# Kernel tuning notes

Measured on AMD Instinct MI355X. Metric: run time of the kernel, lower is better.

## Reference

```python
import jax, jax.numpy as jnp
import numpy as np

BN_EPS = 1e-5

def _bn(x, g, b):
    # BatchNorm1d, training-mode batch statistics
    mu = x.mean(axis=0)
    var = x.var(axis=0)
    return g * (x - mu) / jnp.sqrt(var + BN_EPS) + b

def setup_inputs() -> dict:
    key = jax.random.key(0)
    ks = jax.random.split(key, 10)
    B2, D_in, D1, DIMS, C = 16384, 1024, 512, 256, 40
    B = B2 // 2
    def w(k, shape, fan_in):
        return jax.random.normal(k, shape, jnp.float32) / np.float32(np.sqrt(fan_in))
    return {
        "lufeat": jax.random.normal(ks[0], (B2, D_in), jnp.float32),
        "llabel": jax.random.randint(ks[1], (B,), 0, C),
        "W1": w(ks[2], (D_in, D1), D_in), "b1": jnp.zeros(D1, jnp.float32),
        "W2": w(ks[3], (D1, DIMS), D1), "b2": jnp.zeros(DIMS, jnp.float32),
        "W3": w(ks[4], (DIMS + C, 256), DIMS + C), "b3": jnp.zeros(256, jnp.float32),
        "W4": w(ks[5], (256, 64), 256), "b4": jnp.zeros(64, jnp.float32),
        "W5": w(ks[6], (64, 1), 64), "b5": jnp.zeros(1, jnp.float32),
        "g1": jnp.ones(256, jnp.float32), "be1": jnp.zeros(256, jnp.float32),
        "g2": jnp.ones(64, jnp.float32), "be2": jnp.zeros(64, jnp.float32),
        "mbank0": jax.random.normal(ks[7], (C, DIMS), jnp.float32),
        "start0": jnp.zeros(C, jnp.float32),
    }

def reference(lufeat, llabel, W1, b1, W2, b2, W3, b3, W4, b4, W5, b5,
              g1, be1, g2, be2, mbank0, start0):
    B = lufeat.shape[0] // 2
    h = (lufeat @ W1 + b1) @ W2 + b2            # [2B, dims]
    h = h / jnp.linalg.norm(h, axis=1, keepdims=True)
    lfeat, ufeat = h[:B], h[B:]

    # Sequential per-sample memory-bank scatter/EMA update (detached feats)
    lf_sg = jax.lax.stop_gradient(lfeat)
    def step(carry, xs):
        start, mbank = carry
        lab, feat = xs
        row = jnp.where(start[lab] == 0, feat, 0.9 * mbank[lab] + 0.1 * feat)
        return (start.at[lab].set(1.0), mbank.at[lab].set(row)), None
    (_, mbank), _ = jax.lax.scan(step, (start0, mbank0), (llabel, lf_sg))
    mbank = jax.lax.stop_gradient(mbank)

    # cdist retrieval: [B, C] euclidean distances
    lm = jnp.linalg.norm(lfeat[:, None, :] - mbank[None, :, :], axis=-1)
    lscores = lm.min(axis=-1)
    um = jnp.linalg.norm(ufeat[:, None, :] - mbank[None, :, :], axis=-1)

    uf = jnp.concatenate([ufeat, um], axis=-1)   # [B, dims + C]
    u = jax.nn.relu(_bn(uf @ W3 + b3, g1, be1))
    u = jax.nn.relu(_bn(u @ W4 + b4, g2, be2))   # dropout = identity (eval)
    uscores = u @ W5 + b5                        # [B, 1]
    return lscores, uscores, mbank
```

## Files before the change

kernel.cpp:

```cpp
#include <hip/hip_runtime.h>
#include <hip/hip_bf16.h>
#include <stdint.h>

typedef __attribute__((ext_vector_type(4))) float f32x4;
typedef __attribute__((ext_vector_type(8))) short s16x8;
typedef __attribute__((ext_vector_type(4))) unsigned short u16x4;
typedef __attribute__((ext_vector_type(4))) int i32x4;

#define B2T 16384
#define BH 8192
#define DIN 1024
#define DD1 512
#define DIMS 256
#define NC 40
#define CAPS 2048

__device__ __forceinline__ unsigned short f2b(float f) {
  unsigned int u = __builtin_bit_cast(unsigned int, f);
  u += 0x7FFFu + ((u >> 16) & 1u);
  return (unsigned short)(u >> 16);
}

__device__ __forceinline__ float b2f(unsigned short u) {
  return __builtin_bit_cast(float, ((unsigned int)u) << 16);
}

__device__ __forceinline__ void gload16(const void* g, void* l) {
  __builtin_amdgcn_global_load_lds(
      (const __attribute__((address_space(1))) void*)g,
      (__attribute__((address_space(3))) void*)l, 16, 0, 0);
}

__global__ __launch_bounds__(256) void prep_all(const float* __restrict__ W1,
                                                const float* __restrict__ W2,
                                                const float* __restrict__ b1,
                                                const float* __restrict__ b2,
                                                const float* __restrict__ W3,
                                                const float* __restrict__ W4,
                                                unsigned short* __restrict__ WeffT,
                                                float* __restrict__ beff,
                                                unsigned short* __restrict__ W3T,
                                                unsigned short* __restrict__ W4T,
                                                float* __restrict__ statz) {
  __shared__ float W1s[32][36];
  __shared__ float W2sT[32][36];
  int b = blockIdx.x, t = threadIdx.x;
  if (b < 256) {
    int k0 = (b & 31) * 32, n0 = (b >> 5) * 32;
    int nn = t & 31, kq = t >> 5;
    f32x4 acc = (f32x4){0.f, 0.f, 0.f, 0.f};
    for (int j0 = 0; j0 < DD1; j0 += 32) {
#pragma unroll
      for (int i = 0; i < 4; ++i) {
        int idx = t + 256 * i;
        int kk = idx >> 5, jj = idx & 31;
        W1s[kk][jj] = W1[(size_t)(k0 + kk) * DD1 + j0 + jj];
        W2sT[jj][kk] = W2[(size_t)(j0 + kk) * DIMS + n0 + jj];
      }
      __syncthreads();
#pragma unroll
      for (int jj4 = 0; jj4 < 8; ++jj4) {
        f32x4 w2 = *(const f32x4*)&W2sT[nn][jj4 * 4];
        f32x4 w1_0 = *(const f32x4*)&W1s[kq * 4 + 0][jj4 * 4];
        f32x4 w1_1 = *(const f32x4*)&W1s[kq * 4 + 1][jj4 * 4];
        f32x4 w1_2 = *(const f32x4*)&W1s[kq * 4 + 2][jj4 * 4];
        f32x4 w1_3 = *(const f32x4*)&W1s[kq * 4 + 3][jj4 * 4];
        acc[0] += w1_0[0] * w2[0] + w1_0[1] * w2[1] + w1_0[2] * w2[2] + w1_0[3] * w2[3];
        acc[1] += w1_1[0] * w2[0] + w1_1[1] * w2[1] + w1_1[2] * w2[2] + w1_1[3] * w2[3];
        acc[2] += w1_2[0] * w2[0] + w1_2[1] * w2[1] + w1_2[2] * w2[2] + w1_2[3] * w2[3];
        acc[3] += w1_3[0] * w2[0] + w1_3[1] * w2[1] + w1_3[2] * w2[2] + w1_3[3] * w2[3];
      }
      __syncthreads();
    }
    u16x4 pk = {f2b(acc[0]), f2b(acc[1]), f2b(acc[2]), f2b(acc[3])};
    *(u16x4*)(WeffT + (size_t)(n0 + nn) * DIN + k0 + kq * 4) = pk;
  } else if (b == 256) {
    float a0 = 0.f, a1 = 0.f, a2 = 0.f, a3 = 0.f, a4 = 0.f, a5 = 0.f, a6 = 0.f, a7 = 0.f;
    for (int j = 0; j < DD1; j += 8) {
      a0 += b1[j + 0] * W2[(size_t)(j + 0) * DIMS + t];
      a1 += b1[j + 1] * W2[(size_t)(j + 1) * DIMS + t];
      a2 += b1[j + 2] * W2[(size_t)(j + 2) * DIMS + t];
      a3 += b1[j + 3] * W2[(size_t)(j + 3) * DIMS + t];
      a4 += b1[j + 4] * W2[(size_t)(j + 4) * DIMS + t];
      a5 += b1[j + 5] * W2[(size_t)(j + 5) * DIMS + t];
      a6 += b1[j + 6] * W2[(size_t)(j + 6) * DIMS + t];
      a7 += b1[j + 7] * W2[(size_t)(j + 7) * DIMS + t];
    }
    beff[t] = b2[t] + (((a0 + a1) + (a2 + a3)) + ((a4 + a5) + (a6 + a7)));
  } else if (b < 577) {
    int idx = (b - 257) * 256 + t;
    int n = idx / 320, k = idx - n * 320;
    float v = (k < 296) ? W3[(size_t)k * 256 + n] : 0.0f;
    W3T[(size_t)n * 320 + k] = f2b(v);
  } else if (b < 641) {
    int idx = (b - 577) * 256 + t;
    int n = idx >> 8, k = idx & 255;
    W4T[(size_t)n * 256 + k] = f2b(W4[(size_t)k * 64 + n]);
  } else {
    for (int i = t; i < 640; i += 256) statz[i] = 0.0f;
  }
}

template <int AMODE, int NB, int MI, int CW, int EPI, int K, int TPB>
__global__ __launch_bounds__(TPB) void gemm_core(
    const void* __restrict__ Aptr, int lda, const unsigned short* __restrict__ BT,
    const float* __restrict__ bias, float* __restrict__ C, int ldc,
    float* __restrict__ sums, float* __restrict__ ssqs,
    const float* __restrict__ bnsum, const float* __restrict__ bnssq,
    const float* __restrict__ bng, const float* __restrict__ bnbe,
    unsigned short* __restrict__ uf) {
  constexpr int NW = TPB / 64;
  constexpr int RG = NW / CW;
  constexpr int AR = RG * MI * 16;
  constexpr int ACH = AR * 8;
  constexpr int ABN = (ACH + TPB - 1) / TPB;
  constexpr int BBN = NB * 8 / TPB;
  constexpr int BBUF = NB * 128;
  __shared__ __align__(16) short A_s[2][AR][72];
  __shared__ __align__(16) char B_s[2 * BBUF];
  __shared__ float rs[CW][AR];
  __shared__ float bsc_s[(AMODE == 2) ? 256 : 1];
  __shared__ float bsh_s[(AMODE == 2) ? 256 : 1];
  int t = threadIdx.x;
  int m0 = blockIdx.x * AR;
  int w = t >> 6, lane = t & 63, q = lane >> 4, ln = lane & 15;
  f32x4 acc[MI][4];
#pragma unroll
  for (int mi = 0; mi < MI; ++mi)
#pragma unroll
    for (int ni = 0; ni < 4; ++ni) acc[mi][ni] = (f32x4){0.f, 0.f, 0.f, 0.f};

  f32x4 pa0[ABN][2], pa1[ABN][2];
  s16x8 pab0[ABN], pab1[ABN];

  auto issueA = [&](int kbase, f32x4 (&paX)[ABN][2], s16x8 (&pabX)[ABN]) {
    if (ACH >= TPB || t < ACH) {
#pragma unroll
      for (int i = 0; i < ABN; ++i) {
        int ch = t + TPB * i, row = ch >> 3, kp = (ch & 7) * 8;
        if constexpr (AMODE == 1) {
          const unsigned short* A = (const unsigned short*)Aptr;
          pabX[i] = *(const s16x8*)(A + (size_t)(m0 + row) * lda + kbase + kp);
        } else {
          const float* A = (const float*)Aptr;
          const f32x4* src = (const f32x4*)(A + (size_t)(m0 + row) * lda + kbase + kp);
          paX[i][0] = src[0];
          paX[i][1] = src[1];
        }
      }
    }
  };

  auto gloadB = [&](int kbase, int bufi) {
#pragma unroll
    for (int i = 0; i < BBN; ++i) {
      int ch = t + TPB * i;
      int n = ch >> 3, j = ch & 7;
      int ksw = (j ^ (n & 7)) * 8;
      gload16(BT + (size_t)n * K + kbase + ksw,
              B_s + bufi * BBUF + (w * 64 + TPB * i) * 16);
    }
  };

  auto stageA = [&](int kk, int bufi, f32x4 (&paX)[ABN][2], s16x8 (&pabX)[ABN]) {
    if (ACH >= TPB || t < ACH) {
#pragma unroll
      for (int i = 0; i < ABN; ++i) {
        int ch = t + TPB * i, row = ch >> 3, kp = (ch & 7) * 8;
        if constexpr (AMODE == 1) {
          *(s16x8*)&A_s[bufi][row][kp] = pabX[i];
        } else {
          f32x4 v0 = paX[i][0], v1 = paX[i][1];
          if constexpr (AMODE == 2) {
            float vv[8] = {v0[0], v0[1], v0[2], v0[3], v1[0], v1[1], v1[2], v1[3]};
#pragma unroll
            for (int j = 0; j < 8; ++j) {
              int f = kk + kp + j;
              vv[j] = fmaxf(vv[j] * bsc_s[f] + bsh_s[f], 0.0f);
            }
            v0 = (f32x4){vv[0], vv[1], vv[2], vv[3]};
            v1 = (f32x4){vv[4], vv[5], vv[6], vv[7]};
          }
          s16x8 p;
          p[0] = (short)f2b(v0[0]); p[1] = (short)f2b(v0[1]);
          p[2] = (short)f2b(v0[2]); p[3] = (short)f2b(v0[3]);
          p[4] = (short)f2b(v1[0]); p[5] = (short)f2b(v1[1]);
          p[6] = (short)f2b(v1[2]); p[7] = (short)f2b(v1[3]);
          *(s16x8*)&A_s[bufi][row][kp] = p;
        }
      }
    }
  };

  auto compute = [&](int cur) {
#pragma unroll
    for (int k32 = 0; k32 < 64; k32 += 32) {
      s16x8 af[MI];
      int ab = (w / CW) * MI * 16;
#pragma unroll
      for (int mi = 0; mi < MI; ++mi)
        af[mi] = *(const s16x8*)&A_s[cur][ab + mi * 16 + ln][k32 + q * 8];
      int nb0 = (w % CW) * 64;
#pragma unroll
      for (int ni = 0; ni < 4; ++ni) {
        int brow = nb0 + ni * 16 + ln;
        int bb = (brow * 128 + (k32 + q * 8) * 2) ^ ((brow & 7) << 4);
        s16x8 bfr = *(const s16x8*)(B_s + cur * BBUF + bb);
#pragma unroll
        for (int mi = 0; mi < MI; ++mi)
          acc[mi][ni] = __builtin_amdgcn_mfma_f32_16x16x32_bf16(af[mi], bfr, acc[mi][ni], 0, 0, 0);
      }
    }
  };

  if constexpr (AMODE == 2) {
    if (t < 256) {
      float mu = bnsum[t] * (1.0f / 8192.0f);
      float var = bnssq[t] * (1.0f / 8192.0f) - mu * mu;
      float sc = bng[t] * rsqrtf(var + 1e-5f);
      bsc_s[t] = sc;
      bsh_s[t] = bnbe[t] - mu * sc;
    }
    __syncthreads();
  }

  const int nst = K >> 6;
  issueA(0, pa0, pab0);
  gloadB(0, 0);
  if (nst > 1) issueA(64, pa1, pab1);
  stageA(0, 0, pa0, pab0);
  __syncthreads();

  for (int s = 0; s < nst; s += 2) {
    if (s + 1 < nst) gloadB((s + 1) << 6, 1);
    if (s + 2 < nst) issueA((s + 2) << 6, pa0, pab0);
    compute(0);
    if (s + 1 < nst) stageA((s + 1) << 6, 1, pa1, pab1);
    __syncthreads();
    if (s + 1 < nst) {
      if (s + 2 < nst) gloadB((s + 2) << 6, 0);
      if (s + 3 < nst) issueA((s + 3) << 6, pa1, pab1);
      compute(1);
      if (s + 2 < nst) stageA((s + 2) << 6, 0, pa0, pab0);
      __syncthreads();
    }
  }

  float v[MI][4][4];
#pragma unroll
  for (int mi = 0; mi < MI; ++mi)
#pragma unroll
    for (int ni = 0; ni < 4; ++ni) {
      float bv = bias[(w % CW) * 64 + ni * 16 + ln];
#pragma unroll
      for (int r = 0; r < 4; ++r) v[mi][ni][r] = acc[mi][ni][r] + bv;
    }

  if constexpr (EPI == 1) {
    float p[MI][4];
#pragma unroll
    for (int mi = 0; mi < MI; ++mi)
#pragma unroll
      for (int r = 0; r < 4; ++r) {
        float s = v[mi][0][r] * v[mi][0][r] + v[mi][1][r] * v[mi][1][r] +
                  v[mi][2][r] * v[mi][2][r] + v[mi][3][r] * v[mi][3][r];
        s += __shfl_xor(s, 1); s += __shfl_xor(s, 2);
        s += __shfl_xor(s, 4); s += __shfl_xor(s, 8);
        p[mi][r] = s;
      }
    if (ln == 0) {
#pragma unroll
      for (int mi = 0; mi < MI; ++mi)
#pragma unroll
        for (int r = 0; r < 4; ++r)
          rs[w % CW][(w / CW) * MI * 16 + mi * 16 + q * 4 + r] = p[mi][r];
    }
    __syncthreads();
    if (t < AR) {
      float s = rs[0][t];
#pragma unroll
      for (int i = 1; i < CW; ++i) s += rs[i][t];
      rs[0][t] = rsqrtf(s);
    }
    __syncthreads();
#pragma unroll
    for (int mi = 0; mi < MI; ++mi)
#pragma unroll
      for (int r = 0; r < 4; ++r) {
        int ribf = (w / CW) * MI * 16 + mi * 16 + q * 4 + r;
        float inv = rs[0][ribf];
        int grow = m0 + ribf;
#pragma unroll
        for (int ni = 0; ni < 4; ++ni) {
          int col = (w % CW) * 64 + ni * 16 + ln;
          float nv = v[mi][ni][r] * inv;
          if (grow < BH)
            C[(size_t)grow * ldc + col] = nv;
          else
            uf[(size_t)(grow - BH) * 320 + col] = f2b(nv);
        }
      }
  } else {
#pragma unroll
    for (int mi = 0; mi < MI; ++mi)
#pragma unroll
      for (int ni = 0; ni < 4; ++ni)
#pragma unroll
        for (int r = 0; r < 4; ++r) {
          int grow = m0 + (w / CW) * MI * 16 + mi * 16 + q * 4 + r;
          int col = (w % CW) * 64 + ni * 16 + ln;
          C[(size_t)grow * ldc + col] = v[mi][ni][r];
        }
    if constexpr (EPI == 2 || EPI == 3) {
#pragma unroll
      for (int ni = 0; ni < 4; ++ni) {
        float s = 0.f, s2 = 0.f;
#pragma unroll
        for (int mi = 0; mi < MI; ++mi)
#pragma unroll
          for (int r = 0; r < 4; ++r) {
            float x = v[mi][ni][r];
            s += x; s2 += x * x;
          }
        s += __shfl_xor(s, 16); s += __shfl_xor(s, 32);
        s2 += __shfl_xor(s2, 16); s2 += __shfl_xor(s2, 32);
        if (q == 0) {
          int col = (w % CW) * 64 + ni * 16 + ln;
          atomicAdd(&sums[col], s);
          atomicAdd(&ssqs[col], s2);
        }
      }
    }
  }
}

__global__ __launch_bounds__(256) void bank_kernel(const int* __restrict__ llabel,
                                                   const float* __restrict__ Hn,
                                                   const float* __restrict__ mbank0,
                                                   const float* __restrict__ start0,
                                                   float* __restrict__ mbank_out,
                                                   float* __restrict__ msq) {
  __shared__ i32x4 lab4[BH / 4];
  __shared__ int idx_s[CAPS];
  __shared__ int wcnt[4];
  __shared__ float red[4];
  int t = threadIdx.x, c = blockIdx.x;
  int w = t >> 6, lane = t & 63;

  for (int i = t; i < BH / 4; i += 256) lab4[i] = ((const i32x4*)llabel)[i];
  __syncthreads();
  const int* lab_s = (const int*)lab4;

  int base0 = w * (BH / 4);
  int cnt = 0;
  for (int b = 0; b < BH / 4; b += 64)
    cnt += (int)__popcll(__ballot(lab_s[base0 + b + lane] == c));
  if (lane == 0) wcnt[w] = cnt;
  __syncthreads();
  int off = 0;
#pragma unroll
  for (int i = 0; i < 4; ++i)
    if (i < w) off += wcnt[i];
  int Ktot = wcnt[0] + wcnt[1] + wcnt[2] + wcnt[3];

  int running = off;
  for (int b = 0; b < BH / 4; b += 64) {
    bool hit = lab_s[base0 + b + lane] == c;
    unsigned long long mk = __ballot(hit);
    if (hit) {
      int pos = running + (int)__popcll(mk & ((1ull << lane) - 1ull));
      if (pos < CAPS) idx_s[pos] = base0 + b + lane;
    }
    running += (int)__popcll(mk);
  }
  __syncthreads();
  int K = Ktot < CAPS ? Ktot : CAPS;

  const float l09 = -0.15200309344504997f;
  bool fresh = (start0[c] == 0.0f);
  float out;
  if (K == 0) {
    out = mbank0[(size_t)c * DIMS + t];
  } else {
    float a0 = 0.f, a1 = 0.f, a2 = 0.f, a3 = 0.f, a4 = 0.f, a5 = 0.f, a6 = 0.f, a7 = 0.f;
    float w0fold = fresh ? exp2f((float)K * l09) : 0.f;
    int m = 0;
    for (; m + 8 <= K; m += 8) {
      float e = (float)(K - 1 - m);
      float wa = 0.1f * exp2f(e * l09) + (m == 0 ? w0fold : 0.f);
      a0 += wa * Hn[(size_t)idx_s[m + 0] * DIMS + t];
      a1 += 0.1f * exp2f((e - 1.f) * l09) * Hn[(size_t)idx_s[m + 1] * DIMS + t];
      a2 += 0.1f * exp2f((e - 2.f) * l09) * Hn[(size_t)idx_s[m + 2] * DIMS + t];
      a3 += 0.1f * exp2f((e - 3.f) * l09) * Hn[(size_t)idx_s[m + 3] * DIMS + t];
      a4 += 0.1f * exp2f((e - 4.f) * l09) * Hn[(size_t)idx_s[m + 4] * DIMS + t];
      a5 += 0.1f * exp2f((e - 5.f) * l09) * Hn[(size_t)idx_s[m + 5] * DIMS + t];
      a6 += 0.1f * exp2f((e - 6.f) * l09) * Hn[(size_t)idx_s[m + 6] * DIMS + t];
      a7 += 0.1f * exp2f((e - 7.f) * l09) * Hn[(size_t)idx_s[m + 7] * DIMS + t];
    }
    for (; m < K; ++m) {
      float wa = 0.1f * exp2f((float)(K - 1 - m) * l09) + (m == 0 ? w0fold : 0.f);
      a0 += wa * Hn[(size_t)idx_s[m] * DIMS + t];
    }
    float acc = ((a0 + a1) + (a2 + a3)) + ((a4 + a5) + (a6 + a7));
    float base_v = fresh ? 0.f : exp2f((float)K * l09) * mbank0[(size_t)c * DIMS + t];
    out = acc + base_v;
  }
  mbank_out[(size_t)c * DIMS + t] = out;
  float vv = out * out;
#pragma unroll
  for (int o = 32; o; o >>= 1) vv += __shfl_xor(vv, o);
  if ((t & 63) == 0) red[t >> 6] = vv;
  __syncthreads();
  if (t == 0) msq[c] = (red[0] + red[1]) + (red[2] + red[3]);
}

__global__ __launch_bounds__(256) void dist_kernel(const float* __restrict__ Hn,
                                                   const float* __restrict__ mbank,
                                                   const float* __restrict__ msq,
                                                   float* __restrict__ lscores,
                                                   unsigned short* __restrict__ uf) {
  __shared__ float Ms[NC][260];
  __shared__ float Hs[32][260];
  __shared__ float msq_s[NC];
  int t = threadIdx.x;
  int r0 = blockIdx.x * 32;
  for (int e = t; e < NC * 64; e += 256) {
    int i = e >> 6, d0 = (e & 63) * 4;
    *(f32x4*)&Ms[i][d0] = *(const f32x4*)(mbank + (size_t)i * DIMS + d0);
  }
  if (r0 < BH) {
    for (int e = t; e < 32 * 64; e += 256) {
      int i = e >> 6, d0 = (e & 63) * 4;
      *(f32x4*)&Hs[i][d0] = *(const f32x4*)(Hn + (size_t)(r0 + i) * DIMS + d0);
    }
  } else {
    for (int e = t; e < 32 * 32; e += 256) {
      int i = e >> 5, d0 = (e & 31) * 8;
      s16x8 vb = *(const s16x8*)(uf + (size_t)(r0 - BH + i) * 320 + d0);
#pragma unroll
      for (int j = 0; j < 8; ++j) Hs[i][d0 + j] = b2f((unsigned short)vb[j]);
    }
  }
  if (t < NC) msq_s[t] = msq[t];
  __syncthreads();
  int r = t >> 3, c0 = (t & 7) * 5;
  float g0 = 0, g1 = 0, g2 = 0, g3 = 0, g4 = 0;
  for (int d = 0; d < DIMS; d += 4) {
    f32x4 f = *(const f32x4*)&Hs[r][d];
    f32x4 m0v = *(const f32x4*)&Ms[c0 + 0][d];
    f32x4 m1v = *(const f32x4*)&Ms[c0 + 1][d];
    f32x4 m2v = *(const f32x4*)&Ms[c0 + 2][d];
    f32x4 m3v = *(const f32x4*)&Ms[c0 + 3][d];
    f32x4 m4v = *(const f32x4*)&Ms[c0 + 4][d];
    g0 += f[0] * m0v[0] + f[1] * m0v[1] + f[2] * m0v[2] + f[3] * m0v[3];
    g1 += f[0] * m1v[0] + f[1] * m1v[1] + f[2] * m1v[2] + f[3] * m1v[3];
    g2 += f[0] * m2v[0] + f[1] * m2v[1] + f[2] * m2v[2] + f[3] * m2v[3];
    g3 += f[0] * m3v[0] + f[1] * m3v[1] + f[2] * m3v[2] + f[3] * m3v[3];
    g4 += f[0] * m4v[0] + f[1] * m4v[1] + f[2] * m4v[2] + f[3] * m4v[3];
  }
  int row = r0 + r;
  float d2[5];
  d2[0] = 1.0f + msq_s[c0 + 0] - 2.0f * g0;
  d2[1] = 1.0f + msq_s[c0 + 1] - 2.0f * g1;
  d2[2] = 1.0f + msq_s[c0 + 2] - 2.0f * g2;
  d2[3] = 1.0f + msq_s[c0 + 3] - 2.0f * g3;
  d2[4] = 1.0f + msq_s[c0 + 4] - 2.0f * g4;
  if (row < BH) {
    float mn = fminf(fminf(fminf(d2[0], d2[1]), fminf(d2[2], d2[3])), d2[4]);
    mn = fminf(mn, __shfl_xor(mn, 1, 8));
    mn = fminf(mn, __shfl_xor(mn, 2, 8));
    mn = fminf(mn, __shfl_xor(mn, 4, 8));
    if ((t & 7) == 0) lscores[row] = sqrtf(fmaxf(mn, 0.0f));
  } else {
    unsigned short* dst = uf + (size_t)(row - BH) * 320 + 256 + c0;
#pragma unroll
    for (int qq = 0; qq < 5; ++qq) dst[qq] = f2b(sqrtf(fmaxf(d2[qq], 0.0f)));
  }
}

__global__ __launch_bounds__(256) void uscore_bn(const float* __restrict__ y2,
                                                 const float* __restrict__ sums2,
                                                 const float* __restrict__ ssqs2,
                                                 const float* __restrict__ g2,
                                                 const float* __restrict__ be2,
                                                 const float* __restrict__ W5,
                                                 const float* __restrict__ b5,
                                                 float* __restrict__ out) {
  int t = threadIdx.x;
  int wv = t >> 6, lane = t & 63;
  int row = blockIdx.x * 4 + wv;
  float mu = sums2[lane] * (1.0f / 8192.0f);
  float var = ssqs2[lane] * (1.0f / 8192.0f) - mu * mu;
  float sc = g2[lane] * rsqrtf(var + 1e-5f);
  float sh = be2[lane] - mu * sc;
  float v = fmaxf(y2[(size_t)row * 64 + lane] * sc + sh, 0.0f) * W5[lane];
#pragma unroll
  for (int o = 32; o; o >>= 1) v += __shfl_xor(v, o);
  if (lane == 0) out[row] = v + b5[0];
}

extern "C" void kernel_launch(void* const* d_in, const int* in_sizes, int n_in,
                              void* d_out, int out_size, void* d_ws, size_t ws_size,
                              hipStream_t stream) {
  const float* lufeat = (const float*)d_in[0];
  const int* llabel = (const int*)d_in[1];
  const float* W1 = (const float*)d_in[2];
  const float* b1 = (const float*)d_in[3];
  const float* W2 = (const float*)d_in[4];
  const float* b2 = (const float*)d_in[5];
  const float* W3 = (const float*)d_in[6];
  const float* b3 = (const float*)d_in[7];
  const float* W4 = (const float*)d_in[8];
  const float* b4 = (const float*)d_in[9];
  const float* W5 = (const float*)d_in[10];
  const float* b5 = (const float*)d_in[11];
  const float* g1 = (const float*)d_in[12];
  const float* be1 = (const float*)d_in[13];
  const float* g2 = (const float*)d_in[14];
  const float* be2 = (const float*)d_in[15];
  const float* mbank0 = (const float*)d_in[16];
  const float* start0 = (const float*)d_in[17];

  char* ws = (char*)d_ws;
  unsigned short* WeffT = (unsigned short*)(ws + 0);
  float* Hraw = (float*)(ws + 524288);
  float* ybuf = (float*)(ws + 524288);
  float* y2 = (float*)(ws + 8912896);
  unsigned short* uf = (unsigned short*)(ws + 17301504);
  unsigned short* W3T = (unsigned short*)(ws + 22544384);
  unsigned short* W4T = (unsigned short*)(ws + 22708224);
  float* beff = (float*)(ws + 22740992);
  float* sums1 = (float*)(ws + 22742016);
  float* ssq1 = sums1 + 256;
  float* sums2 = ssq1 + 256;
  float* ssq2 = sums2 + 64;
  float* msq = (float*)(ws + 22744576);

  float* lscores = (float*)d_out;
  float* uscores = lscores + 8192;
  float* mbank = uscores + 8192;

  prep_all<<<642, 256, 0, stream>>>(W1, W2, b1, b2, W3, W4, WeffT, beff, W3T, W4T, sums1);
  gemm_core<0, 256, 2, 4, 1, 1024, 256><<<512, 256, 0, stream>>>(
      lufeat, 1024, WeffT, beff, Hraw, 256,
      nullptr, nullptr, nullptr, nullptr, nullptr, nullptr, uf);
  bank_kernel<<<NC, 256, 0, stream>>>(llabel, Hraw, mbank0, start0, mbank, msq);
  dist_kernel<<<512, 256, 0, stream>>>(Hraw, mbank, msq, lscores, uf);
  gemm_core<1, 256, 1, 4, 2, 320, 512><<<256, 512, 0, stream>>>(
      uf, 320, W3T, b3, ybuf, 256,
      sums1, ssq1, nullptr, nullptr, nullptr, nullptr, nullptr);
  gemm_core<2, 64, 1, 1, 3, 256, 256><<<128, 256, 0, stream>>>(
      ybuf, 256, W4T, b4, y2, 64,
      sums2, ssq2, sums1, ssq1, g1, be1, nullptr);
  uscore_bn<<<2048, 256, 0, stream>>>(y2, sums2, ssq2, g2, be2, W5, b5, uscores);
}
```

Before: 238.0 us.

## Fuse post-GEMM stages into one persistent kernel with software grid barriers

Replaces the bank, distance, W3 GEMM, W4 GEMM and score kernels with a single 512-block persistent kernel that separates phases with an atomic grid barrier. The memory-bank EMA is parallelised over 4 dimension quarters per class, and BatchNorm statistics move from float atomics to per-block partials reduced in a dedicated phase. The aim is to remove several kernel launch gaps and tail effects. In exchange it adds grid-wide spin barriers, and it relies on all 512 blocks being co-resident, which is not guaranteed.

```diff
diff --git a/kernel.cpp b/kernel.cpp
--- a/kernel.cpp
+++ b/kernel.cpp
@@ -14,6 +14,7 @@
 #define DIMS 256
 #define NC 40
 #define CAPS 2048
+#define NBLK 512u
 
 __device__ __forceinline__ unsigned short f2b(float f) {
   unsigned int u = __builtin_bit_cast(unsigned int, f);
@@ -29,6 +30,23 @@
   __builtin_amdgcn_global_load_lds(
       (const __attribute__((address_space(1))) void*)g,
       (__attribute__((address_space(3))) void*)l, 16, 0, 0);
+}
+
+__device__ __forceinline__ void gridbar(unsigned* bar) {
+  __syncthreads();
+  if (threadIdx.x == 0) {
+    unsigned gen = __hip_atomic_load(bar + 1, __ATOMIC_RELAXED, __HIP_MEMORY_SCOPE_AGENT);
+    __threadfence();
+    if (atomicAdd(bar, 1u) == NBLK - 1u) {
+      __hip_atomic_store(bar, 0u, __ATOMIC_RELAXED, __HIP_MEMORY_SCOPE_AGENT);
+      __hip_atomic_store(bar + 1, gen + 1u, __ATOMIC_RELEASE, __HIP_MEMORY_SCOPE_AGENT);
+    } else {
+      while (__hip_atomic_load(bar + 1, __ATOMIC_ACQUIRE, __HIP_MEMORY_SCOPE_AGENT) == gen)
+        __builtin_amdgcn_s_sleep(8);
+    }
+    __threadfence();
+  }
+  __syncthreads();
 }
 
 __global__ __launch_bounds__(256) void prep_all(const float* __restrict__ W1,
@@ -97,7 +115,7 @@
     int n = idx >> 8, k = idx & 255;
     W4T[(size_t)n * 256 + k] = f2b(W4[(size_t)k * 64 + n]);
   } else {
-    for (int i = t; i < 640; i += 256) statz[i] = 0.0f;
+    for (int i = t; i < 688; i += 256) statz[i] = 0.0f;
   }
 }
 
@@ -119,8 +137,6 @@
   __shared__ __align__(16) short A_s[2][AR][72];
   __shared__ __align__(16) char B_s[2 * BBUF];
   __shared__ float rs[CW][AR];
-  __shared__ float bsc_s[(AMODE == 2) ? 256 : 1];
-  __shared__ float bsh_s[(AMODE == 2) ? 256 : 1];
   int t = threadIdx.x;
   int m0 = blockIdx.x * AR;
   int w = t >> 6, lane = t & 63, q = lane >> 4, ln = lane & 15;
@@ -133,7 +149,7 @@
   f32x4 pa0[ABN][2], pa1[ABN][2];
   s16x8 pab0[ABN], pab1[ABN];
 
-  auto issueA = [&](int kbase, f32x4 (&paX)[ABN][2], s16x8 (&pabX)[ABN]) {
+  auto issue = [&](int kbase, f32x4 (&paX)[ABN][2], s16x8 (&pabX)[ABN]) {
     if (ACH >= TPB || t < ACH) {
 #pragma unroll
       for (int i = 0; i < ABN; ++i) {
@@ -162,7 +178,7 @@
     }
   };
 
-  auto stageA = [&](int kk, int bufi, f32x4 (&paX)[ABN][2], s16x8 (&pabX)[ABN]) {
+  auto stage = [&](int bufi, f32x4 (&paX)[ABN][2], s16x8 (&pabX)[ABN]) {
     if (ACH >= TPB || t < ACH) {
 #pragma unroll
       for (int i = 0; i < ABN; ++i) {
@@ -171,16 +187,6 @@
           *(s16x8*)&A_s[bufi][row][kp] = pabX[i];
         } else {
           f32x4 v0 = paX[i][0], v1 = paX[i][1];
-          if constexpr (AMODE == 2) {
-            float vv[8] = {v0[0], v0[1], v0[2], v0[3], v1[0], v1[1], v1[2], v1[3]};
-#pragma unroll
-            for (int j = 0; j < 8; ++j) {
-              int f = kk + kp + j;
-              vv[j] = fmaxf(vv[j] * bsc_s[f] + bsh_s[f], 0.0f);
-            }
-            v0 = (f32x4){vv[0], vv[1], vv[2], vv[3]};
-            v1 = (f32x4){vv[4], vv[5], vv[6], vv[7]};
-          }
           s16x8 p;
           p[0] = (short)f2b(v0[0]); p[1] = (short)f2b(v0[1]);
           p[2] = (short)f2b(v0[2]); p[3] = (short)f2b(v0[3]);
@@ -213,35 +219,24 @@
     }
   };
 
-  if constexpr (AMODE == 2) {
-    if (t < 256) {
-      float mu = bnsum[t] * (1.0f / 8192.0f);
-      float var = bnssq[t] * (1.0f / 8192.0f) - mu * mu;
-      float sc = bng[t] * rsqrtf(var + 1e-5f);
-      bsc_s[t] = sc;
-      bsh_s[t] = bnbe[t] - mu * sc;
-    }
-    __syncthreads();
-  }
-
   const int nst = K >> 6;
-  issueA(0, pa0, pab0);
+  issue(0, pa0, pab0);
   gloadB(0, 0);
-  if (nst > 1) issueA(64, pa1, pab1);
-  stageA(0, 0, pa0, pab0);
+  if (nst > 1) issue(64, pa1, pab1);
+  stage(0, pa0, pab0);
   __syncthreads();
 
   for (int s = 0; s < nst; s += 2) {
     if (s + 1 < nst) gloadB((s + 1) << 6, 1);
-    if (s + 2 < nst) issueA((s + 2) << 6, pa0, pab0);
+    if (s + 2 < nst) issue((s + 2) << 6, pa0, pab0);
     compute(0);
-    if (s + 1 < nst) stageA((s + 1) << 6, 1, pa1, pab1);
+    if (s + 1 < nst) stage(1, pa1, pab1);
     __syncthreads();
     if (s + 1 < nst) {
       if (s + 2 < nst) gloadB((s + 2) << 6, 0);
-      if (s + 3 < nst) issueA((s + 3) << 6, pa1, pab1);
+      if (s + 3 < nst) issue((s + 3) << 6, pa1, pab1);
       compute(1);
-      if (s + 2 < nst) stageA((s + 2) << 6, 0, pa0, pab0);
+      if (s + 2 < nst) stage(0, pa0, pab0);
       __syncthreads();
     }
   }
@@ -300,203 +295,386 @@
             uf[(size_t)(grow - BH) * 320 + col] = f2b(nv);
         }
       }
-  } else {
-#pragma unroll
-    for (int mi = 0; mi < MI; ++mi)
-#pragma unroll
-      for (int ni = 0; ni < 4; ++ni)
-#pragma unroll
-        for (int r = 0; r < 4; ++r) {
-          int grow = m0 + (w / CW) * MI * 16 + mi * 16 + q * 4 + r;
-          int col = (w % CW) * 64 + ni * 16 + ln;
-          C[(size_t)grow * ldc + col] = v[mi][ni][r];
+  }
+}
+
+__global__ __launch_bounds__(256, 2) void fused_back(
+    const int* llabel, const float* Hn, const float* mbank0, const float* start0,
+    float* mbank, float* msq, float* lscores, unsigned short* uf,
+    const unsigned short* W3T, const float* b3, float* ybuf, float* part1,
+    float* bnsc1, float* bnsh1, const float* g1, const float* be1,
+    const unsigned short* W4T, const float* b4, float* y2, float* part2,
+    float* bnsc2, float* bnsh2, const float* g2, const float* be2,
+    const float* W5, const float* b5, float* uscores, unsigned* bar) {
+  __shared__ __align__(16) char smem[75264];
+  const int t = threadIdx.x;
+  const int w = t >> 6, lane = t & 63, q = lane >> 4, ln = lane & 15;
+  const int bx = blockIdx.x;
+  const float l09 = -0.15200309344504997f;
+
+  if (bx < 160) {
+    int c = bx >> 2, dq = bx & 3;
+    int* lab_s = (int*)smem;
+    int* idx_s = (int*)(smem + 32768);
+    float* redp = (float*)(smem + 40960);
+    int* wcnt = (int*)(smem + 41984);
+    for (int i = t; i < BH / 4; i += 256) ((i32x4*)lab_s)[i] = ((const i32x4*)llabel)[i];
+    __syncthreads();
+    int base0 = w * (BH / 4);
+    int cnt = 0;
+    for (int b = 0; b < BH / 4; b += 64)
+      cnt += (int)__popcll(__ballot(lab_s[base0 + b + lane] == c));
+    if (lane == 0) wcnt[w] = cnt;
+    __syncthreads();
+    int off = 0;
+#pragma unroll
+    for (int i = 0; i < 4; ++i)
+      if (i < w) off += wcnt[i];
+    int Ktot = wcnt[0] + wcnt[1] + wcnt[2] + wcnt[3];
+    int running = off;
+    for (int b = 0; b < BH / 4; b += 64) {
+      bool hit = lab_s[base0 + b + lane] == c;
+      unsigned long long mk = __ballot(hit);
+      if (hit) {
+        int pos = running + (int)__popcll(mk & ((1ull << lane) - 1ull));
+        if (pos < CAPS) idx_s[pos] = base0 + b + lane;
+      }
+      running += (int)__popcll(mk);
+    }
+    __syncthreads();
+    int K = Ktot < CAPS ? Ktot : CAPS;
+    bool fresh = (start0[c] == 0.0f);
+    int dcol = t & 63, rr = t >> 6;
+    int d = dq * 64 + dcol;
+    float p0 = 0.f, p1 = 0.f, p2 = 0.f, p3 = 0.f;
+    if (K > 0) {
+      float w0fold = fresh ? exp2f((float)K * l09) : 0.f;
+      int m = rr;
+      for (; m + 12 < K; m += 16) {
+        float e = (float)(K - 1 - m);
+        float wa = 0.1f * exp2f(e * l09) + (m == 0 ? w0fold : 0.f);
+        p0 += wa * Hn[(size_t)idx_s[m] * DIMS + d];
+        p1 += 0.1f * exp2f((e - 4.f) * l09) * Hn[(size_t)idx_s[m + 4] * DIMS + d];
+        p2 += 0.1f * exp2f((e - 8.f) * l09) * Hn[(size_t)idx_s[m + 8] * DIMS + d];
+        p3 += 0.1f * exp2f((e - 12.f) * l09) * Hn[(size_t)idx_s[m + 12] * DIMS + d];
+      }
+      for (; m < K; m += 4) {
+        float wa = 0.1f * exp2f((float)(K - 1 - m) * l09) + (m == 0 ? w0fold : 0.f);
+        p0 += wa * Hn[(size_t)idx_s[m] * DIMS + d];
+      }
+    }
+    redp[rr * 64 + dcol] = (p0 + p1) + (p2 + p3);
+    __syncthreads();
+    if (t < 64) {
+      int dd = dq * 64 + t;
+      float out;
+      if (K == 0) {
+        out = mbank0[(size_t)c * DIMS + dd];
+      } else {
+        float base_v = fresh ? 0.f : exp2f((float)K * l09) * mbank0[(size_t)c * DIMS + dd];
+        out = ((redp[t] + redp[64 + t]) + (redp[128 + t] + redp[192 + t])) + base_v;
+      }
+      mbank[(size_t)c * DIMS + dd] = out;
+      float vv = out * out;
+#pragma unroll
+      for (int o = 32; o; o >>= 1) vv += __shfl_xor(vv, o);
+      if (t == 0) atomicAdd(&msq[c], vv);
+    }
+  }
+  gridbar(bar);
+
+  {
+    float* Ms = (float*)smem;
+    float* Hs = (float*)(smem + 41600);
+    float* msq_s = (float*)(smem + 74880);
+    int r0 = bx * 32;
+    for (int e = t; e < NC * 64; e += 256) {
+      int i = e >> 6, d0 = (e & 63) * 4;
+      *(f32x4*)&Ms[i * 260 + d0] = *(const f32x4*)(mbank + (size_t)i * DIMS + d0);
+    }
+    if (r0 < BH) {
+      for (int e = t; e < 32 * 64; e += 256) {
+        int i = e >> 6, d0 = (e & 63) * 4;
+        *(f32x4*)&Hs[i * 260 + d0] = *(const f32x4*)(Hn + (size_t)(r0 + i) * DIMS + d0);
+      }
+    } else {
+      for (int e = t; e < 32 * 32; e += 256) {
+        int i = e >> 5, d0 = (e & 31) * 8;
+        s16x8 vb = *(const s16x8*)(uf + (size_t)(r0 - BH + i) * 320 + d0);
+#pragma unroll
+        for (int jj = 0; jj < 8; ++jj) Hs[i * 260 + d0 + jj] = b2f((unsigned short)vb[jj]);
+      }
+    }
+    if (t < NC) msq_s[t] = msq[t];
+    __syncthreads();
+    int r = t >> 3, c0 = (t & 7) * 5;
+    float g0 = 0, g1v = 0, g2v = 0, g3 = 0, g4 = 0;
+    for (int d = 0; d < DIMS; d += 4) {
+      f32x4 f = *(const f32x4*)&Hs[r * 260 + d];
+      f32x4 m0v = *(const f32x4*)&Ms[(c0 + 0) * 260 + d];
+      f32x4 m1v = *(const f32x4*)&Ms[(c0 + 1) * 260 + d];
+      f32x4 m2v = *(const f32x4*)&Ms[(c0 + 2) * 260 + d];
+      f32x4 m3v = *(const f32x4*)&Ms[(c0 + 3) * 260 + d];
+      f32x4 m4v = *(const f32x4*)&Ms[(c0 + 4) * 260 + d];
+      g0 += f[0] * m0v[0] + f[1] * m0v[1] + f[2] * m0v[2] + f[3] * m0v[3];
+      g1v += f[0] * m1v[0] + f[1] * m1v[1] + f[2] * m1v[2] + f[3] * m1v[3];
+      g2v += f[0] * m2v[0] + f[1] * m2v[1] + f[2] * m2v[2] + f[3] * m2v[3];
+      g3 += f[0] * m3v[0] + f[1] * m3v[1] + f[2] * m3v[2] + f[3] * m3v[3];
+      g4 += f[0] * m4v[0] + f[1] * m4v[1] + f[2] * m4v[2] + f[3] * m4v[3];
+    }
+    int row = r0 + r;
+    float d2[5];
+    d2[0] = 1.0f + msq_s[c0 + 0] - 2.0f * g0;
+    d2[1] = 1.0f + msq_s[c0 + 1] - 2.0f * g1v;
+    d2[2] = 1.0f + msq_s[c0 + 2] - 2.0f * g2v;
+    d2[3] = 1.0f + msq_s[c0 + 3] - 2.0f * g3;
+    d2[4] = 1.0f + msq_s[c0 + 4] - 2.0f * g4;
+    if (row < BH) {
+      float mn = fminf(fminf(fminf(d2[0], d2[1]), fminf(d2[2], d2[3])), d2[4]);
+      mn = fminf(mn, __shfl_xor(mn, 1, 8));
+      mn = fminf(mn, __shfl_xor(mn, 2, 8));
+      mn = fminf(mn, __shfl_xor(mn, 4, 8));
+      if ((t & 7) == 0) lscores[row] = sqrtf(fmaxf(mn, 0.0f));
+    } else {
+      unsigned short* dst = uf + (size_t)(row - BH) * 320 + 256 + c0;
+#pragma unroll
+      for (int qq = 0; qq < 5; ++qq) dst[qq] = f2b(sqrtf(fmaxf(d2[qq], 0.0f)));
+    }
+  }
+  gridbar(bar);
+
+  {
+    short* A_s = (short*)smem;
+    char* Bb = smem + 4608;
+    int m0 = bx * 16;
+    f32x4 acc[4];
+#pragma unroll
+    for (int ni = 0; ni < 4; ++ni) acc[ni] = (f32x4){0.f, 0.f, 0.f, 0.f};
+    s16x8 pA0, pA1;
+    auto issueA2 = [&](int kbase, s16x8& p) {
+      if (t < 128) {
+        int row = t >> 3, kp = (t & 7) * 8;
+        p = *(const s16x8*)(uf + (size_t)(m0 + row) * 320 + kbase + kp);
+      }
+    };
+    auto stageA2 = [&](int bufi, s16x8& p) {
+      if (t < 128) {
+        int row = t >> 3, kp = (t & 7) * 8;
+        *(s16x8*)&A_s[(bufi * 16 + row) * 72 + kp] = p;
+      }
+    };
+    auto gloadB2 = [&](int kbase, int bufi) {
+#pragma unroll
+      for (int i = 0; i < 8; ++i) {
+        int ch = t + 256 * i;
+        int n = ch >> 3, j = ch & 7;
+        int ksw = (j ^ (n & 7)) * 8;
+        gload16(W3T + (size_t)n * 320 + kbase + ksw, Bb + bufi * 32768 + ch * 16);
+      }
+    };
+    auto compute2 = [&](int cur) {
+#pragma unroll
+      for (int k32 = 0; k32 < 64; k32 += 32) {
+        s16x8 af = *(const s16x8*)&A_s[(cur * 16 + ln) * 72 + k32 + q * 8];
+#pragma unroll
+        for (int ni = 0; ni < 4; ++ni) {
+          int brow = w * 64 + ni * 16 + ln;
+          int bb = (brow * 128 + (k32 + q * 8) * 2) ^ ((brow & 7) << 4);
+          s16x8 bfr = *(const s16x8*)(Bb + cur * 32768 + bb);
+          acc[ni] = __builtin_amdgcn_mfma_f32_16x16x32_bf16(af, bfr, acc[ni], 0, 0, 0);
         }
-    if constexpr (EPI == 2 || EPI == 3) {
-#pragma unroll
-      for (int ni = 0; ni < 4; ++ni) {
-        float s = 0.f, s2 = 0.f;
-#pragma unroll
-        for (int mi = 0; mi < MI; ++mi)
-#pragma unroll
-          for (int r = 0; r < 4; ++r) {
-            float x = v[mi][ni][r];
-            s += x; s2 += x * x;
-          }
-        s += __shfl_xor(s, 16); s += __shfl_xor(s, 32);
-        s2 += __shfl_xor(s2, 16); s2 += __shfl_xor(s2, 32);
-        if (q == 0) {
-          int col = (w % CW) * 64 + ni * 16 + ln;
-          atomicAdd(&sums[col], s);
-          atomicAdd(&ssqs[col], s2);
+      }
+    };
+    issueA2(0, pA0); gloadB2(0, 0); issueA2(64, pA1); stageA2(0, pA0);
+    __syncthreads();
+    for (int s = 0; s < 5; s += 2) {
+      if (s + 1 < 5) gloadB2((s + 1) << 6, 1);
+      if (s + 2 < 5) issueA2((s + 2) << 6, pA0);
+      compute2(0);
+      if (s + 1 < 5) stageA2(1, pA1);
+      __syncthreads();
+      if (s + 1 < 5) {
+        if (s + 2 < 5) gloadB2((s + 2) << 6, 0);
+        if (s + 3 < 5) issueA2((s + 3) << 6, pA1);
+        compute2(1);
+        if (s + 2 < 5) stageA2(0, pA0);
+        __syncthreads();
+      }
+    }
+#pragma unroll
+    for (int ni = 0; ni < 4; ++ni) {
+      int col = w * 64 + ni * 16 + ln;
+      float bv = b3[col];
+      float s = 0.f, s2 = 0.f;
+#pragma unroll
+      for (int r = 0; r < 4; ++r) {
+        float x = acc[ni][r] + bv;
+        ybuf[(size_t)(m0 + q * 4 + r) * 256 + col] = x;
+        s += x; s2 += x * x;
+      }
+      s += __shfl_xor(s, 16); s += __shfl_xor(s, 32);
+      s2 += __shfl_xor(s2, 16); s2 += __shfl_xor(s2, 32);
+      if (q == 0) {
+        part1[col * 512 + bx] = s;
+        part1[131072 + col * 512 + bx] = s2;
+      }
+    }
+  }
+  gridbar(bar);
+
+  if (bx < 256) {
+    float* red = (float*)smem;
+    float s = part1[bx * 512 + t] + part1[bx * 512 + 256 + t];
+    float s2 = part1[131072 + bx * 512 + t] + part1[131072 + bx * 512 + 256 + t];
+#pragma unroll
+    for (int o = 32; o; o >>= 1) { s += __shfl_xor(s, o); s2 += __shfl_xor(s2, o); }
+    if (lane == 0) { red[w] = s; red[4 + w] = s2; }
+    __syncthreads();
+    if (t == 0) {
+      float S = (red[0] + red[1]) + (red[2] + red[3]);
+      float S2 = (red[4] + red[5]) + (red[6] + red[7]);
+      float mu = S * (1.0f / 8192.0f);
+      float var = S2 * (1.0f / 8192.0f) - mu * mu;
+      float sc = g1[bx] * rsqrtf(var + 1e-5f);
+      bnsc1[bx] = sc;
+      bnsh1[bx] = be1[bx] - mu * sc;
+    }
+  }
+  gridbar(bar);
+
+  if (bx < 128) {
+    short* A_s = (short*)smem;
+    char* Bb = smem + 18432;
+    float* bsc_s = (float*)(smem + 34816);
+    float* bsh_s = (float*)(smem + 35840);
+    bsc_s[t] = bnsc1[t];
+    bsh_s[t] = bnsh1[t];
+    __syncthreads();
+    int m0 = bx * 64;
+    f32x4 acc[4];
+#pragma unroll
+    for (int ni = 0; ni < 4; ++ni) acc[ni] = (f32x4){0.f, 0.f, 0.f, 0.f};
+    f32x4 pa0[2][2], pa1[2][2];
+    auto issueA3 = [&](int kbase, f32x4 (&pa)[2][2]) {
+#pragma unroll
+      for (int i = 0; i < 2; ++i) {
+        int ch = t + 256 * i, row = ch >> 3, kp = (ch & 7) * 8;
+        const f32x4* src = (const f32x4*)(ybuf + (size_t)(m0 + row) * 256 + kbase + kp);
+        pa[i][0] = src[0];
+        pa[i][1] = src[1];
+      }
+    };
+    auto stageA3 = [&](int kbase, int bufi, f32x4 (&pa)[2][2]) {
+#pragma unroll
+      for (int i = 0; i < 2; ++i) {
+        int ch = t + 256 * i, row = ch >> 3, kp = (ch & 7) * 8;
+        float vv[8] = {pa[i][0][0], pa[i][0][1], pa[i][0][2], pa[i][0][3],
+                       pa[i][1][0], pa[i][1][1], pa[i][1][2], pa[i][1][3]};
+#pragma unroll
+        for (int j = 0; j < 8; ++j) {
+          int f = kbase + kp + j;
+          vv[j] = fmaxf(vv[j] * bsc_s[f] + bsh_s[f], 0.0f);
         }
-      }
-    }
-  }
-}
-
-__global__ __launch_bounds__(256) void bank_kernel(const int* __restrict__ llabel,
-                                                   const float* __restrict__ Hn,
-                                                   const float* __restrict__ mbank0,
-                                                   const float* __restrict__ start0,
-                                                   float* __restrict__ mbank_out,
-                                                   float* __restrict__ msq) {
-  __shared__ i32x4 lab4[BH / 4];
-  __shared__ int idx_s[CAPS];
-  __shared__ int wcnt[4];
-  __shared__ float red[4];
-  int t = threadIdx.x, c = blockIdx.x;
-  int w = t >> 6, lane = t & 63;
-
-  for (int i = t; i < BH / 4; i += 256) lab4[i] = ((const i32x4*)llabel)[i];
-  __syncthreads();
-  const int* lab_s = (const int*)lab4;
-
-  int base0 = w * (BH / 4);
-  int cnt = 0;
-  for (int b = 0; b < BH / 4; b += 64)
-    cnt += (int)__popcll(__ballot(lab_s[base0 + b + lane] == c));
-  if (lane == 0) wcnt[w] = cnt;
-  __syncthreads();
-  int off = 0;
-#pragma unroll
-  for (int i = 0; i < 4; ++i)
-    if (i < w) off += wcnt[i];
-  int Ktot = wcnt[0] + wcnt[1] + wcnt[2] + wcnt[3];
-
-  int running = off;
-  for (int b = 0; b < BH / 4; b += 64) {
-    bool hit = lab_s[base0 + b + lane] == c;
-    unsigned long long mk = __ballot(hit);
-    if (hit) {
-      int pos = running + (int)__popcll(mk & ((1ull << lane) - 1ull));
-      if (pos < CAPS) idx_s[pos] = base0 + b + lane;
-    }
-    running += (int)__popcll(mk);
-  }
-  __syncthreads();
-  int K = Ktot < CAPS ? Ktot : CAPS;
-
-  const float l09 = -0.15200309344504997f;
-  bool fresh = (start0[c] == 0.0f);
-  float out;
-  if (K == 0) {
-    out = mbank0[(size_t)c * DIMS + t];
-  } else {
-    float a0 = 0.f, a1 = 0.f, a2 = 0.f, a3 = 0.f, a4 = 0.f, a5 = 0.f, a6 = 0.f, a7 = 0.f;
-    float w0fold = fresh ? exp2f((float)K * l09) : 0.f;
-    int m = 0;
-    for (; m + 8 <= K; m += 8) {
-      float e = (float)(K - 1 - m);
-      float wa = 0.1f * exp2f(e * l09) + (m == 0 ? w0fold : 0.f);
-      a0 += wa * Hn[(size_t)idx_s[m + 0] * DIMS + t];
-      a1 += 0.1f * exp2f((e - 1.f) * l09) * Hn[(size_t)idx_s[m + 1] * DIMS + t];
-      a2 += 0.1f * exp2f((e - 2.f) * l09) * Hn[(size_t)idx_s[m + 2] * DIMS + t];
-      a3 += 0.1f * exp2f((e - 3.f) * l09) * Hn[(size_t)idx_s[m + 3] * DIMS + t];
-      a4 += 0.1f * exp2f((e - 4.f) * l09) * Hn[(size_t)idx_s[m + 4] * DIMS + t];
-      a5 += 0.1f * exp2f((e - 5.f) * l09) * Hn[(size_t)idx_s[m + 5] * DIMS + t];
-      a6 += 0.1f * exp2f((e - 6.f) * l09) * Hn[(size_t)idx_s[m + 6] * DIMS + t];
-      a7 += 0.1f * exp2f((e - 7.f) * l09) * Hn[(size_t)idx_s[m + 7] * DIMS + t];
-    }
-    for (; m < K; ++m) {
-      float wa = 0.1f * exp2f((float)(K - 1 - m) * l09) + (m == 0 ? w0fold : 0.f);
-      a0 += wa * Hn[(size_t)idx_s[m] * DIMS + t];
-    }
-    float acc = ((a0 + a1) + (a2 + a3)) + ((a4 + a5) + (a6 + a7));
-    float base_v = fresh ? 0.f : exp2f((float)K * l09) * mbank0[(size_t)c * DIMS + t];
-    out = acc + base_v;
-  }
-  mbank_out[(size_t)c * DIMS + t] = out;
-  float vv = out * out;
-#pragma unroll
-  for (int o = 32; o; o >>= 1) vv += __shfl_xor(vv, o);
-  if ((t & 63) == 0) red[t >> 6] = vv;
-  __syncthreads();
-  if (t == 0) msq[c] = (red[0] + red[1]) + (red[2] + red[3]);
-}
-
-__global__ __launch_bounds__(256) void dist_kernel(const float* __restrict__ Hn,
-                                                   const float* __restrict__ mbank,
-                                                   const float* __restrict__ msq,
-                                                   float* __restrict__ lscores,
-                                                   unsigned short* __restrict__ uf) {
-  __shared__ float Ms[NC][260];
-  __shared__ float Hs[32][260];
-  __shared__ float msq_s[NC];
-  int t = threadIdx.x;
-  int r0 = blockIdx.x * 32;
-  for (int e = t; e < NC * 64; e += 256) {
-    int i = e >> 6, d0 = (e & 63) * 4;
-    *(f32x4*)&Ms[i][d0] = *(const f32x4*)(mbank + (size_t)i * DIMS + d0);
-  }
-  if (r0 < BH) {
-    for (int e = t; e < 32 * 64; e += 256) {
-      int i = e >> 6, d0 = (e & 63) * 4;
-      *(f32x4*)&Hs[i][d0] = *(const f32x4*)(Hn + (size_t)(r0 + i) * DIMS + d0);
-    }
-  } else {
-    for (int e = t; e < 32 * 32; e += 256) {
-      int i = e >> 5, d0 = (e & 31) * 8;
-      s16x8 vb = *(const s16x8*)(uf + (size_t)(r0 - BH + i) * 320 + d0);
-#pragma unroll
-      for (int j = 0; j < 8; ++j) Hs[i][d0 + j] = b2f((unsigned short)vb[j]);
-    }
-  }
-  if (t < NC) msq_s[t] = msq[t];
-  __syncthreads();
-  int r = t >> 3, c0 = (t & 7) * 5;
-  float g0 = 0, g1 = 0, g2 = 0, g3 = 0, g4 = 0;
-  for (int d = 0; d < DIMS; d += 4) {
-    f32x4 f = *(const f32x4*)&Hs[r][d];
-    f32x4 m0v = *(const f32x4*)&Ms[c0 + 0][d];
-    f32x4 m1v = *(const f32x4*)&Ms[c0 + 1][d];
-    f32x4 m2v = *(const f32x4*)&Ms[c0 + 2][d];
-    f32x4 m3v = *(const f32x4*)&Ms[c0 + 3][d];
-    f32x4 m4v = *(const f32x4*)&Ms[c0 + 4][d];
-    g0 += f[0] * m0v[0] + f[1] * m0v[1] + f[2] * m0v[2] + f[3] * m0v[3];
-    g1 += f[0] * m1v[0] + f[1] * m1v[1] + f[2] * m1v[2] + f[3] * m1v[3];
-    g2 += f[0] * m2v[0] + f[1] * m2v[1] + f[2] * m2v[2] + f[3] * m2v[3];
-    g3 += f[0] * m3v[0] + f[1] * m3v[1] + f[2] * m3v[2] + f[3] * m3v[3];
-    g4 += f[0] * m4v[0] + f[1] * m4v[1] + f[2] * m4v[2] + f[3] * m4v[3];
-  }
-  int row = r0 + r;
-  float d2[5];
-  d2[0] = 1.0f + msq_s[c0 + 0] - 2.0f * g0;
-  d2[1] = 1.0f + msq_s[c0 + 1] - 2.0f * g1;
-  d2[2] = 1.0f + msq_s[c0 + 2] - 2.0f * g2;
-  d2[3] = 1.0f + msq_s[c0 + 3] - 2.0f * g3;
-  d2[4] = 1.0f + msq_s[c0 + 4] - 2.0f * g4;
-  if (row < BH) {
-    float mn = fminf(fminf(fminf(d2[0], d2[1]), fminf(d2[2], d2[3])), d2[4]);
-    mn = fminf(mn, __shfl_xor(mn, 1, 8));
-    mn = fminf(mn, __shfl_xor(mn, 2, 8));
-    mn = fminf(mn, __shfl_xor(mn, 4, 8));
-    if ((t & 7) == 0) lscores[row] = sqrtf(fmaxf(mn, 0.0f));
-  } else {
-    unsigned short* dst = uf + (size_t)(row - BH) * 320 + 256 + c0;
-#pragma unroll
-    for (int qq = 0; qq < 5; ++qq) dst[qq] = f2b(sqrtf(fmaxf(d2[qq], 0.0f)));
-  }
-}
-
-__global__ __launch_bounds__(256) void uscore_bn(const float* __restrict__ y2,
-                                                 const float* __restrict__ sums2,
-                                                 const float* __restrict__ ssqs2,
-                                                 const float* __restrict__ g2,
-                                                 const float* __restrict__ be2,
-                                                 const float* __restrict__ W5,
-                                                 const float* __restrict__ b5,
-                                                 float* __restrict__ out) {
-  int t = threadIdx.x;
-  int wv = t >> 6, lane = t & 63;
-  int row = blockIdx.x * 4 + wv;
-  float mu = sums2[lane] * (1.0f / 8192.0f);
-  float var = ssqs2[lane] * (1.0f / 8192.0f) - mu * mu;
-  float sc = g2[lane] * rsqrtf(var + 1e-5f);
-  float sh = be2[lane] - mu * sc;
-  float v = fmaxf(y2[(size_t)row * 64 + lane] * sc + sh, 0.0f) * W5[lane];
-#pragma unroll
-  for (int o = 32; o; o >>= 1) v += __shfl_xor(v, o);
-  if (lane == 0) out[row] = v + b5[0];
+        s16x8 p;
+        p[0] = (short)f2b(vv[0]); p[1] = (short)f2b(vv[1]);
+        p[2] = (short)f2b(vv[2]); p[3] = (short)f2b(vv[3]);
+        p[4] = (short)f2b(vv[4]); p[5] = (short)f2b(vv[5]);
+        p[6] = (short)f2b(vv[6]); p[7] = (short)f2b(vv[7]);
+        *(s16x8*)&A_s[(bufi * 64 + row) * 72 + kp] = p;
+      }
+    };
+    auto gloadB3 = [&](int kbase, int bufi) {
+#pragma unroll
+      for (int i = 0; i < 2; ++i) {
+        int ch = t + 256 * i, n = ch >> 3, j = ch & 7;
+        int ksw = (j ^ (n & 7)) * 8;
+        gload16(W4T + (size_t)n * 256 + kbase + ksw, Bb + bufi * 8192 + ch * 16);
+      }
+    };
+    auto compute3 = [&](int cur) {
+#pragma unroll
+      for (int k32 = 0; k32 < 64; k32 += 32) {
+        s16x8 af = *(const s16x8*)&A_s[(cur * 64 + w * 16 + ln) * 72 + k32 + q * 8];
+#pragma unroll
+        for (int ni = 0; ni < 4; ++ni) {
+          int brow = ni * 16 + ln;
+          int bb = (brow * 128 + (k32 + q * 8) * 2) ^ ((brow & 7) << 4);
+          s16x8 bfr = *(const s16x8*)(Bb + cur * 8192 + bb);
+          acc[ni] = __builtin_amdgcn_mfma_f32_16x16x32_bf16(af, bfr, acc[ni], 0, 0, 0);
+        }
+      }
+    };
+    issueA3(0, pa0); gloadB3(0, 0); issueA3(64, pa1); stageA3(0, 0, pa0);
+    __syncthreads();
+    for (int s = 0; s < 4; s += 2) {
+      if (s + 1 < 4) gloadB3((s + 1) << 6, 1);
+      if (s + 2 < 4) issueA3((s + 2) << 6, pa0);
+      compute3(0);
+      if (s + 1 < 4) stageA3((s + 1) << 6, 1, pa1);
+      __syncthreads();
+      if (s + 1 < 4) {
+        if (s + 2 < 4) gloadB3((s + 2) << 6, 0);
+        if (s + 3 < 4) issueA3((s + 3) << 6, pa1);
+        compute3(1);
+        if (s + 2 < 4) stageA3((s + 2) << 6, 0, pa0);
+        __syncthreads();
+      }
+    }
+#pragma unroll
+    for (int ni = 0; ni < 4; ++ni) {
+      int col = ni * 16 + ln;
+      float bv = b4[col];
+      float s = 0.f, s2 = 0.f;
+#pragma unroll
+      for (int r = 0; r < 4; ++r) {
+        float x = acc[ni][r] + bv;
+        y2[(size_t)(m0 + w * 16 + q * 4 + r) * 64 + col] = x;
+        s += x; s2 += x * x;
+      }
+      s += __shfl_xor(s, 16); s += __shfl_xor(s, 32);
+      s2 += __shfl_xor(s2, 16); s2 += __shfl_xor(s2, 32);
+      if (q == 0) {
+        part2[col * 512 + bx * 4 + w] = s;
+        part2[32768 + col * 512 + bx * 4 + w] = s2;
+      }
+    }
+  }
+  gridbar(bar);
+
+  if (bx < 64) {
+    float* red = (float*)smem;
+    float s = part2[bx * 512 + t] + part2[bx * 512 + 256 + t];
+    float s2 = part2[32768 + bx * 512 + t] + part2[32768 + bx * 512 + 256 + t];
+#pragma unroll
+    for (int o = 32; o; o >>= 1) { s += __shfl_xor(s, o); s2 += __shfl_xor(s2, o); }
+    if (lane == 0) { red[w] = s; red[4 + w] = s2; }
+    __syncthreads();
+    if (t == 0) {
+      float S = (red[0] + red[1]) + (red[2] + red[3]);
+      float S2 = (red[4] + red[5]) + (red[6] + red[7]);
+      float mu = S * (1.0f / 8192.0f);
+      float var = S2 * (1.0f / 8192.0f) - mu * mu;
+      float sc = g2[bx] * rsqrtf(var + 1e-5f);
+      bnsc2[bx] = sc;
+      bnsh2[bx] = be2[bx] - mu * sc;
+    }
+  }
+  gridbar(bar);
+
+  {
+    float sc = bnsc2[lane];
+    float sh = bnsh2[lane];
+    float w5 = W5[lane];
+    float bb5 = b5[0];
+#pragma unroll
+    for (int i = 0; i < 4; ++i) {
+      int row = bx * 16 + w * 4 + i;
+      float v = fmaxf(y2[(size_t)row * 64 + lane] * sc + sh, 0.0f) * w5;
+#pragma unroll
+      for (int o = 32; o; o >>= 1) v += __shfl_xor(v, o);
+      if (lane == 0) uscores[row] = v + bb5;
+    }
+  }
 }
 
 extern "C" void kernel_launch(void* const* d_in, const int* in_sizes, int n_in,
@@ -530,27 +708,27 @@
   unsigned short* W3T = (unsigned short*)(ws + 22544384);
   unsigned short* W4T = (unsigned short*)(ws + 22708224);
   float* beff = (float*)(ws + 22740992);
-  float* sums1 = (float*)(ws + 22742016);
-  float* ssq1 = sums1 + 256;
-  float* sums2 = ssq1 + 256;
-  float* ssq2 = sums2 + 64;
+  float* statz = (float*)(ws + 22742016);
   float* msq = (float*)(ws + 22744576);
+  unsigned* bar = (unsigned*)(ws + 22744736);
+  float* part1 = (float*)(ws + 22745088);
+  float* part2 = (float*)(ws + 23793664);
+  float* bnsc1 = (float*)(ws + 24055808);
+  float* bnsh1 = (float*)(ws + 24056832);
+  float* bnsc2 = (float*)(ws + 24057856);
+  float* bnsh2 = (float*)(ws + 24058112);
 
   float* lscores = (float*)d_out;
   float* uscores = lscores + 8192;
   float* mbank = uscores + 8192;
 
-  prep_all<<<642, 256, 0, stream>>>(W1, W2, b1, b2, W3, W4, WeffT, beff, W3T, W4T, sums1);
+  prep_all<<<642, 256, 0, stream>>>(W1, W2, b1, b2, W3, W4, WeffT, beff, W3T, W4T, statz);
   gemm_core<0, 256, 2, 4, 1, 1024, 256><<<512, 256, 0, stream>>>(
       lufeat, 1024, WeffT, beff, Hraw, 256,
       nullptr, nullptr, nullptr, nullptr, nullptr, nullptr, uf);
-  bank_kernel<<<NC, 256, 0, stream>>>(llabel, Hraw, mbank0, start0, mbank, msq);
-  dist_kernel<<<512, 256, 0, stream>>>(Hraw, mbank, msq, lscores, uf);
-  gemm_core<1, 256, 1, 4, 2, 320, 512><<<256, 512, 0, stream>>>(
-      uf, 320, W3T, b3, ybuf, 256,
-      sums1, ssq1, nullptr, nullptr, nullptr, nullptr, nullptr);
-  gemm_core<2, 64, 1, 1, 3, 256, 256><<<128, 256, 0, stream>>>(
-      ybuf, 256, W4T, b4, y2, 64,
-      sums2, ssq2, sums1, ssq1, g1, be1, nullptr);
-  uscore_bn<<<2048, 256, 0, stream>>>(y2, sums2, ssq2, g2, be2, W5, b5, uscores);
+  fused_back<<<512, 256, 0, stream>>>(
+      llabel, Hraw, mbank0, start0, mbank, msq, lscores, uf,
+      W3T, b3, ybuf, part1, bnsc1, bnsh1, g1, be1,
+      W4T, b4, y2, part2, bnsc2, bnsh2, g2, be2,
+      W5, b5, uscores, bar);
 }
```

Measured after the change: 614.3 us. 158% more time.
